# Kernel optimization log

Measured on AMD Instinct MI355X. Metric: run time of the kernel, lower is better.

## Reference

```python
import jax, jax.numpy as jnp
import numpy as np
from jax import lax

B, N, D = 16, 2048, 256
H = 64  # hidden_dim
EPS = 1e-5


def zero_softmax(x, eps=EPS):
    # zeros stay exactly zero: exp(0)-1 == 0
    e = jnp.exp(x) - 1.0
    return e / (jnp.sum(e, axis=-1, keepdims=True) + eps)


def setup_inputs() -> dict:
    key = jax.random.key(0)
    ks = jax.random.split(key, 9)
    s_in = 1.0 / np.sqrt(D)
    x = jax.random.normal(ks[0], (B, N, D), dtype=jnp.float32)
    Wq = jax.random.uniform(ks[1], (D, H), jnp.float32, -s_in, s_in)
    bq = jax.random.uniform(ks[2], (H,), jnp.float32, -s_in, s_in)
    Wk = jax.random.uniform(ks[3], (D, H), jnp.float32, -s_in, s_in)
    bk = jax.random.uniform(ks[4], (H,), jnp.float32, -s_in, s_in)
    Wv = jax.random.uniform(ks[5], (D, H), jnp.float32, -s_in, s_in)
    bv = jax.random.uniform(ks[6], (H,), jnp.float32, -s_in, s_in)
    s_c = 1.0 / 3.0  # conv fan_in = 1*3*3 = 9
    conv_w = jax.random.uniform(ks[7], (1, 1, 3, 3), jnp.float32, -s_c, s_c)
    conv_b = jax.random.uniform(ks[8], (1,), jnp.float32, -s_c, s_c)
    return {"x": x, "Wq": Wq, "bq": bq, "Wk": Wk, "bk": bk,
            "Wv": Wv, "bv": bv, "conv_w": conv_w, "conv_b": conv_b}


def reference(x, Wq, bq, Wk, bk, Wv, bv, conv_w, conv_b):
    scale = H ** (-0.5)
    q = jnp.einsum('bnd,dh->bnh', x, Wq) + bq
    k = jnp.einsum('bnd,dh->bnh', x, Wk) + bk
    v = jnp.einsum('bnd,dh->bnh', x, Wv) + bv
    A_dense = jnp.einsum('bnh,bmh->bnm', q, k) * scale  # [B, N, N]
    A_in = A_dense[:, None, :, :]  # [B, 1, N, N]
    A_conv = lax.conv_general_dilated(
        A_in, conv_w, window_strides=(1, 1), padding='SAME',
        dimension_numbers=('NCHW', 'OIHW', 'NCHW')) + conv_b[None, :, None, None]
    A_conv = jax.nn.sigmoid(A_conv)[:, 0, :, :]
    A_sparse = jax.nn.relu(A_dense - A_conv)
    A_norm = zero_softmax(A_sparse)
    return jnp.einsum('bnm,bmh->bnh', A_norm, v)
```

## Files before the change

### kernel.cpp

```cpp
#include <hip/hip_runtime.h>
#include <hip/hip_bf16.h>

typedef __bf16 bf16_t;
typedef __bf16 bf16x8 __attribute__((ext_vector_type(8)));
typedef float  floatx4 __attribute__((ext_vector_type(4)));

#define BQ 16
#define NTOK 2048
#define DIM 256
#define HD 64

__global__ __launch_bounds__(256) void k_prep(const float* __restrict__ Wq,
                                              const float* __restrict__ Wk,
                                              const float* __restrict__ Wv,
                                              bf16_t* __restrict__ wt,
                                              float* __restrict__ outz,
                                              float* __restrict__ rsz) {
    int o = blockIdx.x * 256 + threadIdx.x;
    if (o < 49152) {
        int w = o >> 14;
        int r = o & 16383;
        int h = r >> 8;
        int d = r & 255;
        const float* W = (w == 0) ? Wq : ((w == 1) ? Wk : Wv);
        wt[o] = (bf16_t)W[d * 64 + h];
    }
    float4 z = make_float4(0.f, 0.f, 0.f, 0.f);
    for (int u = o; u < 532480; u += 262144) {
        if (u < 524288) ((float4*)outz)[u] = z;
        else            ((float4*)rsz)[u - 524288] = z;
    }
}

#define XS 264
__global__ __launch_bounds__(256) void k_qkv(const float* __restrict__ x,
                                             const bf16_t* __restrict__ wt,
                                             const float* __restrict__ bq,
                                             const float* __restrict__ bk,
                                             const float* __restrict__ bv,
                                             bf16_t* __restrict__ qb,
                                             bf16_t* __restrict__ kb,
                                             bf16_t* __restrict__ vt) {
    __shared__ bf16_t x_ls[64 * XS];
    __shared__ bf16_t vt_ls[64 * 72];

    int b  = blockIdx.x >> 5;
    int t0 = (blockIdx.x & 31) << 6;
    int t  = threadIdx.x;
    int lane = t & 63;
    int w    = t >> 6;
    int m_   = lane & 15;
    int q4   = lane >> 4;

    for (int tau = t; tau < 4096; tau += 256) {
        int row = tau >> 6, ch = tau & 63;
        float4 v = ((const float4*)x)[(size_t)(b * NTOK + t0 + row) * 64 + ch];
        bf16_t tmp[4] = {(bf16_t)v.x, (bf16_t)v.y, (bf16_t)v.z, (bf16_t)v.w};
        *(uint2*)(&x_ls[row * XS + ch * 4]) = *(uint2*)tmp;
    }
    __syncthreads();

    for (int wi = 0; wi < 3; ++wi) {
        const bf16_t* wtw = wt + wi * 16384;
        floatx4 acc[4];
        #pragma unroll
        for (int mt = 0; mt < 4; ++mt) acc[mt] = floatx4{0.f, 0.f, 0.f, 0.f};

        #pragma unroll
        for (int ks = 0; ks < 8; ++ks) {
            bf16x8 bfrag = *(const bf16x8*)(wtw + (16 * w + m_) * 256 + ks * 32 + q4 * 8);
            #pragma unroll
            for (int mt = 0; mt < 4; ++mt) {
                bf16x8 afrag = *(const bf16x8*)(&x_ls[(16 * mt + m_) * XS + ks * 32 + q4 * 8]);
                acc[mt] = __builtin_amdgcn_mfma_f32_16x16x32_bf16(afrag, bfrag, acc[mt], 0, 0, 0);
            }
        }
        const float* bias_p = (wi == 0) ? bq : ((wi == 1) ? bk : bv);
        float bias = bias_p[16 * w + m_];
        float scale = (wi == 0) ? 0.125f : 1.0f;

        if (wi < 2) {
            bf16_t* dst = (wi == 0) ? qb : kb;
            #pragma unroll
            for (int mt = 0; mt < 4; ++mt)
                #pragma unroll
                for (int r = 0; r < 4; ++r) {
                    int tok = t0 + 16 * mt + 4 * q4 + r;
                    dst[(size_t)(b * NTOK + tok) * 64 + 16 * w + m_] = (bf16_t)((acc[mt][r] + bias) * scale);
                }
        } else {
            #pragma unroll
            for (int mt = 0; mt < 4; ++mt)
                #pragma unroll
                for (int r = 0; r < 4; ++r)
                    vt_ls[(16 * w + m_) * 72 + 16 * mt + 4 * q4 + r] = (bf16_t)(acc[mt][r] + bias);
            __syncthreads();
            for (int tau = t; tau < 512; tau += 256) {
                int h = tau >> 3, ch = tau & 7;
                uint4 val = *(const uint4*)(&vt_ls[h * 72 + ch * 8]);
                *(uint4*)(vt + (size_t)(b * 64 + h) * NTOK + t0 + ch * 8) = val;
            }
        }
    }
}

#define SA 68
#define SP 72
#define RINT 62
#define L2E 1.44269504f

static __device__ __forceinline__ bf16x8 as_bf16x8(uint4 u) {
    union { uint4 a; bf16x8 b; } c; c.a = u; return c.b;
}

__global__ __launch_bounds__(512) void k_attn(const bf16_t* __restrict__ qb,
                                              const bf16_t* __restrict__ kb,
                                              const bf16_t* __restrict__ vt,
                                              const float* __restrict__ conv_w,
                                              const float* __restrict__ conv_b,
                                              float* __restrict__ outp,
                                              float* __restrict__ rsg) {
    __shared__ bf16_t k_ls[64 * SP];
    __shared__ bf16_t v_ls[64 * SP];
    __shared__ bf16_t p_ls[64 * SP];
    __shared__ float  A_ls[64 * SA];

    int b  = blockIdx.z;
    int r0 = blockIdx.x * RINT;
    int it_beg = (int)(blockIdx.y * 34) >> 2;
    int it_end = (int)((blockIdx.y + 1) * 34) >> 2;

    int t = threadIdx.x, lane = t & 63, w = t >> 6;
    int m_ = lane & 15, q4 = lane >> 4;
    int wtj = w & 3;
    int wti = (w >> 2) << 1;

    const uint* vt32 = (const uint*)vt + (size_t)b * 64 * 1024;

    uint4 kreg;
    uint  vreg[4];
    auto prefetch = [&](int c0) {
        {
            int row = t >> 3, ch = t & 7;
            int g = c0 - 1 + row;
            uint4 val = make_uint4(0u, 0u, 0u, 0u);
            if (g >= 0 && g < NTOK)
                val = *(const uint4*)(kb + (size_t)(b * NTOK + g) * 64 + ch * 8);
            kreg = val;
        }
        #pragma unroll
        for (int j = 0; j < 4; ++j) {
            int tau = t + 512 * j;
            int n = c0 + 2 * (tau & 31);
            uint val = 0u;
            if (n < NTOK) val = vt32[(tau >> 5) * 1024 + (n >> 1)];
            vreg[j] = val;
        }
    };

    prefetch(it_beg * RINT);

    float cw[9];
    #pragma unroll
    for (int i = 0; i < 9; ++i) cw[i] = conv_w[i] * L2E;
    float cb = conv_b[0] * L2E;

    bf16x8 qreg[2][2];
    #pragma unroll
    for (int p = 0; p < 2; ++p) {
        int g = r0 - 1 + 16 * (wti + p) + m_;
        #pragma unroll
        for (int ks = 0; ks < 2; ++ks) {
            uint4 val = make_uint4(0u, 0u, 0u, 0u);
            if (g >= 0 && g < NTOK)
                val = *(const uint4*)(qb + (size_t)(b * NTOK + g) * 64 + ks * 32 + q4 * 8);
            qreg[p][ks] = as_bf16x8(val);
        }
    }

    for (int u = t; u < 2304; u += 512) ((uint*)p_ls)[u] = 0u;
    if (t < 256) A_ls[(t >> 2) * SA + 64 + (t & 3)] = 0.f;

    floatx4 accO[2];
    accO[0] = floatx4{0.f, 0.f, 0.f, 0.f};
    accO[1] = floatx4{0.f, 0.f, 0.f, 0.f};
    float rs[2] = {0.f, 0.f};

    int i0 = (t >> 4) + 1;
    int gq = t & 15;
    int cvoff = (i0 - 1) * SA + 4 * gq;
    bool gq15 = (gq == 15);

    for (int itg = it_beg; itg < it_end; ++itg) {
        {
            int row = t >> 3, ch = t & 7;
            *(uint4*)(&k_ls[row * SP + ch * 8]) = kreg;
            #pragma unroll
            for (int j = 0; j < 4; ++j) {
                int tau = t + 512 * j;
                *(uint*)(&v_ls[(tau >> 5) * SP + 2 * (tau & 31)]) = vreg[j];
            }
        }
        __syncthreads();

        #pragma unroll
        for (int p = 0; p < 2; ++p) {
            floatx4 a = floatx4{0.f, 0.f, 0.f, 0.f};
            #pragma unroll
            for (int ks = 0; ks < 2; ++ks) {
                bf16x8 bfr = *(const bf16x8*)(&k_ls[(16 * wtj + m_) * SP + ks * 32 + q4 * 8]);
                a = __builtin_amdgcn_mfma_f32_16x16x32_bf16(qreg[p][ks], bfr, a, 0, 0, 0);
            }
            int rbase = 16 * (wti + p) + 4 * q4;
            #pragma unroll
            for (int r = 0; r < 4; ++r)
                A_ls[(rbase + r) * SA + 16 * wtj + m_] = a[r];
        }
        __syncthreads();

        if (itg + 1 < it_end) prefetch((itg + 1) * RINT);

        #pragma unroll
        for (int round = 0; round < 2; ++round) {
            if (round == 0 || t < 480) {
                const float* base = &A_ls[cvoff + round * (32 * SA)];
                float a0[6], a1[6], a2[6];
                *(float4*)(a0)     = *(const float4*)(base);
                *(float2*)(a0 + 4) = *(const float2*)(base + 4);
                *(float4*)(a1)     = *(const float4*)(base + SA);
                *(float2*)(a1 + 4) = *(const float2*)(base + SA + 4);
                *(float4*)(a2)     = *(const float4*)(base + 2 * SA);
                *(float2*)(a2 + 4) = *(const float2*)(base + 2 * SA + 4);
                float esum = 0.f;
                bf16_t quad[4];
                #pragma unroll
                for (int x = 0; x < 4; ++x) {
                    float conv = cb
                        + cw[0] * a0[x] + cw[1] * a0[x + 1] + cw[2] * a0[x + 2]
                        + cw[3] * a1[x] + cw[4] * a1[x + 1] + cw[5] * a1[x + 2]
                        + cw[6] * a2[x] + cw[7] * a2[x + 1] + cw[8] * a2[x + 2];
                    float sig = __builtin_amdgcn_rcpf(1.f + __builtin_amdgcn_exp2f(-conv));
                    float s = fmaxf(a1[x + 1] - sig, 0.f);
                    float ev = __builtin_amdgcn_exp2f(s * L2E) - 1.f;
                    if (x >= 2) ev = gq15 ? 0.f : ev;
                    quad[x] = (bf16_t)ev;
                    esum += ev;
                }
                rs[round] += esum;
                *(uint2*)(&p_ls[(i0 + round * 32) * SP + 4 * gq]) = *(uint2*)quad;
            }
        }
        __syncthreads();

        #pragma unroll
        for (int ks = 0; ks < 2; ++ks) {
            bf16x8 bfr = *(const bf16x8*)(&v_ls[(16 * wtj + m_) * SP + ks * 32 + q4 * 8]);
            #pragma unroll
            for (int p = 0; p < 2; ++p) {
                bf16x8 af = *(const bf16x8*)(&p_ls[(16 * (wti + p) + m_) * SP + ks * 32 + q4 * 8]);
                accO[p] = __builtin_amdgcn_mfma_f32_16x16x32_bf16(af, bfr, accO[p], 0, 0, 0);
            }
        }
        __syncthreads();
    }

    float s0 = rs[0], s1 = rs[1];
    #pragma unroll
    for (int d = 1; d < 16; d <<= 1) {
        s0 += __shfl_xor(s0, d);
        s1 += __shfl_xor(s1, d);
    }
    if ((t & 15) == 0) {
        int g0 = r0 + i0 - 1;
        if (g0 < NTOK) atomicAdd(&rsg[b * NTOK + g0], s0);
        if (t < 480 && g0 + 32 < NTOK) atomicAdd(&rsg[b * NTOK + g0 + 32], s1);
    }

    #pragma unroll
    for (int p = 0; p < 2; ++p) {
        int rbase = 16 * (wti + p) + 4 * q4;
        #pragma unroll
        for (int r = 0; r < 4; ++r) {
            int i = rbase + r;
            int grow = r0 + i - 1;
            if (i >= 1 && i < 63 && grow < NTOK)
                atomicAdd(&outp[((size_t)(b * NTOK + grow) << 6) + 16 * wtj + m_], accO[p][r]);
        }
    }
}

__global__ __launch_bounds__(256) void k_norm(float* __restrict__ out,
                                              const float* __restrict__ rsg) {
    int gid = blockIdx.x * 256 + threadIdx.x;
    float4 o = ((float4*)out)[gid];
    float d = rsg[gid >> 4] + 1e-5f;
    float inv = 1.f / d;
    o.x *= inv; o.y *= inv; o.z *= inv; o.w *= inv;
    ((float4*)out)[gid] = o;
}

extern "C" void kernel_launch(void* const* d_in, const int* in_sizes, int n_in,
                              void* d_out, int out_size, void* d_ws, size_t ws_size,
                              hipStream_t stream) {
    const float* x  = (const float*)d_in[0];
    const float* Wq = (const float*)d_in[1];
    const float* bq = (const float*)d_in[2];
    const float* Wk = (const float*)d_in[3];
    const float* bk = (const float*)d_in[4];
    const float* Wv = (const float*)d_in[5];
    const float* bv = (const float*)d_in[6];
    const float* cw = (const float*)d_in[7];
    const float* cb = (const float*)d_in[8];
    float* out = (float*)d_out;

    char* ws = (char*)d_ws;
    bf16_t* wt = (bf16_t*)ws;
    bf16_t* qb = (bf16_t*)(ws + 98304);
    bf16_t* kb = (bf16_t*)(ws + 98304 + 4194304);
    bf16_t* vt = (bf16_t*)(ws + 98304 + 8388608);
    float*  rsg = (float*)(ws + 98304 + 12582912);

    k_prep<<<dim3(1024), dim3(256), 0, stream>>>(Wq, Wk, Wv, wt, out, rsg);
    k_qkv<<<dim3(512), dim3(256), 0, stream>>>(x, wt, bq, bk, bv, qb, kb, vt);
    k_attn<<<dim3(34, 4, BQ), dim3(512), 0, stream>>>(qb, kb, vt, cw, cb, out, rsg);
    k_norm<<<dim3(2048), dim3(256), 0, stream>>>(out, rsg);
}
```

Baseline: 201.7 us.

## Double-buffer K tiles, fuse conv rows, drop a barrier, split columns three ways

The K tile is now double-buffered in shared memory. K and V for the next iterations are stored right after the first barrier, which removes the trailing per-iteration __syncthreads. The conv/sigmoid stage now has each thread compute two adjacent rows, reusing the shared middle rows of the 3x3 stencil and cutting LDS reads. The V load pattern is reshaped into a single uint4 store per thread. The column split across blockIdx.y changes from 4 to 3, so there are fewer blocks and fewer atomic partial writes, at the cost of less parallelism and longer per-block loops.

```diff
diff --git a/kernel.cpp b/kernel.cpp
--- a/kernel.cpp
+++ b/kernel.cpp
@@ -120,15 +120,16 @@
                                               const float* __restrict__ conv_b,
                                               float* __restrict__ outp,
                                               float* __restrict__ rsg) {
-    __shared__ bf16_t k_ls[64 * SP];
+    __shared__ bf16_t k_ls[2][64 * SP];
     __shared__ bf16_t v_ls[64 * SP];
     __shared__ bf16_t p_ls[64 * SP];
     __shared__ float  A_ls[64 * SA];
 
     int b  = blockIdx.z;
     int r0 = blockIdx.x * RINT;
-    int it_beg = (int)(blockIdx.y * 34) >> 2;
-    int it_end = (int)((blockIdx.y + 1) * 34) >> 2;
+    int cy = blockIdx.y;
+    int it_beg = (cy * 34) / 3;
+    int it_end = ((cy + 1) * 34) / 3;
 
     int t = threadIdx.x, lane = t & 63, w = t >> 6;
     int m_ = lane & 15, q4 = lane >> 4;
@@ -136,34 +137,37 @@
     int wti = (w >> 2) << 1;
 
     const uint* vt32 = (const uint*)vt + (size_t)b * 64 * 1024;
+    const bf16_t* kb_b = kb + (size_t)b * NTOK * 64;
+
+    int krow = t >> 3, kch = t & 7;
 
     uint4 kreg;
     uint  vreg[4];
-    auto prefetch = [&](int c0) {
-        {
-            int row = t >> 3, ch = t & 7;
-            int g = c0 - 1 + row;
-            uint4 val = make_uint4(0u, 0u, 0u, 0u);
-            if (g >= 0 && g < NTOK)
-                val = *(const uint4*)(kb + (size_t)(b * NTOK + g) * 64 + ch * 8);
-            kreg = val;
-        }
+
+    auto load_k = [&](int c0) {
+        int g = c0 - 1 + krow;
+        uint4 val = make_uint4(0u, 0u, 0u, 0u);
+        if (g >= 0 && g < NTOK)
+            val = *(const uint4*)(kb_b + (size_t)g * 64 + kch * 8);
+        kreg = val;
+    };
+    auto load_v = [&](int c0) {
+        int cb2 = (c0 >> 1) + 4 * kch;
         #pragma unroll
         for (int j = 0; j < 4; ++j) {
-            int tau = t + 512 * j;
-            int n = c0 + 2 * (tau & 31);
             uint val = 0u;
-            if (n < NTOK) val = vt32[(tau >> 5) * 1024 + (n >> 1)];
+            if (cb2 + j < 1024) val = vt32[krow * 1024 + cb2 + j];
             vreg[j] = val;
         }
     };
 
-    prefetch(it_beg * RINT);
+    load_k(it_beg * RINT);
+    load_v(it_beg * RINT);
 
     float cw[9];
     #pragma unroll
     for (int i = 0; i < 9; ++i) cw[i] = conv_w[i] * L2E;
-    float cb = conv_b[0] * L2E;
+    float cbv = conv_b[0] * L2E;
 
     bf16x8 qreg[2][2];
     #pragma unroll
@@ -181,74 +185,82 @@
     for (int u = t; u < 2304; u += 512) ((uint*)p_ls)[u] = 0u;
     if (t < 256) A_ls[(t >> 2) * SA + 64 + (t & 3)] = 0.f;
 
+    *(uint4*)(&k_ls[0][krow * SP + kch * 8]) = kreg;
+    load_k((it_beg + 1) * RINT);
+
     floatx4 accO[2];
     accO[0] = floatx4{0.f, 0.f, 0.f, 0.f};
     accO[1] = floatx4{0.f, 0.f, 0.f, 0.f};
     float rs[2] = {0.f, 0.f};
 
-    int i0 = (t >> 4) + 1;
+    int u2 = t >> 4;
     int gq = t & 15;
-    int cvoff = (i0 - 1) * SA + 4 * gq;
     bool gq15 = (gq == 15);
+    int ci = 2 * u2 + 1;
+    const float* cbase = &A_ls[(ci - 1) * SA + 4 * gq];
+
+    __syncthreads();
 
     for (int itg = it_beg; itg < it_end; ++itg) {
+        int rel = (itg - it_beg) & 1;
+        const bf16_t* kcur = k_ls[rel];
+
         {
-            int row = t >> 3, ch = t & 7;
-            *(uint4*)(&k_ls[row * SP + ch * 8]) = kreg;
-            #pragma unroll
-            for (int j = 0; j < 4; ++j) {
-                int tau = t + 512 * j;
-                *(uint*)(&v_ls[(tau >> 5) * SP + 2 * (tau & 31)]) = vreg[j];
+            bf16x8 bfr0 = *(const bf16x8*)(&kcur[(16 * wtj + m_) * SP + q4 * 8]);
+            bf16x8 bfr1 = *(const bf16x8*)(&kcur[(16 * wtj + m_) * SP + 32 + q4 * 8]);
+            #pragma unroll
+            for (int p = 0; p < 2; ++p) {
+                floatx4 a = floatx4{0.f, 0.f, 0.f, 0.f};
+                a = __builtin_amdgcn_mfma_f32_16x16x32_bf16(qreg[p][0], bfr0, a, 0, 0, 0);
+                a = __builtin_amdgcn_mfma_f32_16x16x32_bf16(qreg[p][1], bfr1, a, 0, 0, 0);
+                int rbase = 16 * (wti + p) + 4 * q4;
+                #pragma unroll
+                for (int r = 0; r < 4; ++r)
+                    A_ls[(rbase + r) * SA + 16 * wtj + m_] = a[r];
             }
         }
         __syncthreads();
 
-        #pragma unroll
-        for (int p = 0; p < 2; ++p) {
-            floatx4 a = floatx4{0.f, 0.f, 0.f, 0.f};
-            #pragma unroll
-            for (int ks = 0; ks < 2; ++ks) {
-                bf16x8 bfr = *(const bf16x8*)(&k_ls[(16 * wtj + m_) * SP + ks * 32 + q4 * 8]);
-                a = __builtin_amdgcn_mfma_f32_16x16x32_bf16(qreg[p][ks], bfr, a, 0, 0, 0);
-            }
-            int rbase = 16 * (wti + p) + 4 * q4;
-            #pragma unroll
-            for (int r = 0; r < 4; ++r)
-                A_ls[(rbase + r) * SA + 16 * wtj + m_] = a[r];
-        }
-        __syncthreads();
-
-        if (itg + 1 < it_end) prefetch((itg + 1) * RINT);
-
-        #pragma unroll
-        for (int round = 0; round < 2; ++round) {
-            if (round == 0 || t < 480) {
-                const float* base = &A_ls[cvoff + round * (32 * SA)];
-                float a0[6], a1[6], a2[6];
-                *(float4*)(a0)     = *(const float4*)(base);
-                *(float2*)(a0 + 4) = *(const float2*)(base + 4);
-                *(float4*)(a1)     = *(const float4*)(base + SA);
-                *(float2*)(a1 + 4) = *(const float2*)(base + SA + 4);
-                *(float4*)(a2)     = *(const float4*)(base + 2 * SA);
-                *(float2*)(a2 + 4) = *(const float2*)(base + 2 * SA + 4);
-                float esum = 0.f;
-                bf16_t quad[4];
-                #pragma unroll
-                for (int x = 0; x < 4; ++x) {
-                    float conv = cb
-                        + cw[0] * a0[x] + cw[1] * a0[x + 1] + cw[2] * a0[x + 2]
-                        + cw[3] * a1[x] + cw[4] * a1[x + 1] + cw[5] * a1[x + 2]
-                        + cw[6] * a2[x] + cw[7] * a2[x + 1] + cw[8] * a2[x + 2];
-                    float sig = __builtin_amdgcn_rcpf(1.f + __builtin_amdgcn_exp2f(-conv));
-                    float s = fmaxf(a1[x + 1] - sig, 0.f);
-                    float ev = __builtin_amdgcn_exp2f(s * L2E) - 1.f;
-                    if (x >= 2) ev = gq15 ? 0.f : ev;
-                    quad[x] = (bf16_t)ev;
-                    esum += ev;
-                }
-                rs[round] += esum;
-                *(uint2*)(&p_ls[(i0 + round * 32) * SP + 4 * gq]) = *(uint2*)quad;
-            }
+        *(uint4*)(&k_ls[rel ^ 1][krow * SP + kch * 8]) = kreg;
+        *(uint4*)(&v_ls[krow * SP + 8 * kch]) = make_uint4(vreg[0], vreg[1], vreg[2], vreg[3]);
+        load_k((itg + 2) * RINT);
+        load_v((itg + 1) * RINT);
+
+        if (u2 < 31) {
+            float a0[6], a1[6], a2[6], a3[6];
+            *(float4*)(a0)     = *(const float4*)(cbase);
+            *(float2*)(a0 + 4) = *(const float2*)(cbase + 4);
+            *(float4*)(a1)     = *(const float4*)(cbase + SA);
+            *(float2*)(a1 + 4) = *(const float2*)(cbase + SA + 4);
+            *(float4*)(a2)     = *(const float4*)(cbase + 2 * SA);
+            *(float2*)(a2 + 4) = *(const float2*)(cbase + 2 * SA + 4);
+            *(float4*)(a3)     = *(const float4*)(cbase + 3 * SA);
+            *(float2*)(a3 + 4) = *(const float2*)(cbase + 3 * SA + 4);
+            float es0 = 0.f, es1 = 0.f;
+            bf16_t q0[4], q1[4];
+            #pragma unroll
+            for (int x = 0; x < 4; ++x) {
+                float c0v = cbv
+                    + cw[0] * a0[x] + cw[1] * a0[x + 1] + cw[2] * a0[x + 2]
+                    + cw[3] * a1[x] + cw[4] * a1[x + 1] + cw[5] * a1[x + 2]
+                    + cw[6] * a2[x] + cw[7] * a2[x + 1] + cw[8] * a2[x + 2];
+                float c1v = cbv
+                    + cw[0] * a1[x] + cw[1] * a1[x + 1] + cw[2] * a1[x + 2]
+                    + cw[3] * a2[x] + cw[4] * a2[x + 1] + cw[5] * a2[x + 2]
+                    + cw[6] * a3[x] + cw[7] * a3[x + 1] + cw[8] * a3[x + 2];
+                float sig0 = __builtin_amdgcn_rcpf(1.f + __builtin_amdgcn_exp2f(-c0v));
+                float sig1 = __builtin_amdgcn_rcpf(1.f + __builtin_amdgcn_exp2f(-c1v));
+                float s0 = fmaxf(a1[x + 1] - sig0, 0.f);
+                float s1 = fmaxf(a2[x + 1] - sig1, 0.f);
+                float e0 = __builtin_amdgcn_exp2f(s0 * L2E) - 1.f;
+                float e1 = __builtin_amdgcn_exp2f(s1 * L2E) - 1.f;
+                if (x >= 2) { e0 = gq15 ? 0.f : e0; e1 = gq15 ? 0.f : e1; }
+                q0[x] = (bf16_t)e0; q1[x] = (bf16_t)e1;
+                es0 += e0; es1 += e1;
+            }
+            rs[0] += es0; rs[1] += es1;
+            *(uint2*)(&p_ls[ci * SP + 4 * gq])       = *(uint2*)q0;
+            *(uint2*)(&p_ls[(ci + 1) * SP + 4 * gq]) = *(uint2*)q1;
         }
         __syncthreads();
 
@@ -261,7 +273,6 @@
                 accO[p] = __builtin_amdgcn_mfma_f32_16x16x32_bf16(af, bfr, accO[p], 0, 0, 0);
             }
         }
-        __syncthreads();
     }
 
     float s0 = rs[0], s1 = rs[1];
@@ -270,10 +281,10 @@
         s0 += __shfl_xor(s0, d);
         s1 += __shfl_xor(s1, d);
     }
-    if ((t & 15) == 0) {
-        int g0 = r0 + i0 - 1;
-        if (g0 < NTOK) atomicAdd(&rsg[b * NTOK + g0], s0);
-        if (t < 480 && g0 + 32 < NTOK) atomicAdd(&rsg[b * NTOK + g0 + 32], s1);
+    if ((t & 15) == 0 && u2 < 31) {
+        int gr = r0 + 2 * u2;
+        if (gr < NTOK)     atomicAdd(&rsg[b * NTOK + gr],     s0);
+        if (gr + 1 < NTOK) atomicAdd(&rsg[b * NTOK + gr + 1], s1);
     }
 
     #pragma unroll
@@ -322,6 +333,6 @@
 
     k_prep<<<dim3(1024), dim3(256), 0, stream>>>(Wq, Wk, Wv, wt, out, rsg);
     k_qkv<<<dim3(512), dim3(256), 0, stream>>>(x, wt, bq, bk, bv, qb, kb, vt);
-    k_attn<<<dim3(34, 4, BQ), dim3(512), 0, stream>>>(qb, kb, vt, cw, cb, out, rsg);
+    k_attn<<<dim3(34, 3, BQ), dim3(512), 0, stream>>>(qb, kb, vt, cw, cb, out, rsg);
     k_norm<<<dim3(2048), dim3(256), 0, stream>>>(out, rsg);
 }
```

Result: no change. 201.9 us (+0.1%).
